# Kernel optimization log

Measured on AMD Instinct MI355X. Metric: run time of the kernel, lower is better.

The kernel has to match this reference:

```python
import jax, jax.numpy as jnp
import numpy as np

EPS = 0.5  # energy-relaxation learning rate (epsilon in __init__)


def rho(s):
    return jnp.clip(s, 0.0, 1.0)


def setup_inputs() -> dict:
    key = jax.random.key(0)
    k_x, k_w1, k_w2 = jax.random.split(key, 3)
    B, I, H, O = 8192, 1024, 128, 1000
    x = jax.random.uniform(k_x, (B, I), dtype=jnp.float32)
    hidden0 = jnp.zeros((B, H), dtype=jnp.float32)
    output0 = jnp.zeros((B, O), dtype=jnp.float32)
    b_in = jnp.zeros((I,), dtype=jnp.float32)
    b_h = jnp.zeros((H,), dtype=jnp.float32)
    b_o = jnp.zeros((O,), dtype=jnp.float32)
    # xavier_uniform: U(-a, a), a = sqrt(6 / (fan_in + fan_out))
    a1 = np.sqrt(6.0 / (I + H)).astype(np.float32)
    a2 = np.sqrt(6.0 / (H + O)).astype(np.float32)
    W1 = jax.random.uniform(k_w1, (I, H), minval=-a1, maxval=a1, dtype=jnp.float32)
    W2 = jax.random.uniform(k_w2, (H, O), minval=-a2, maxval=a2, dtype=jnp.float32)
    return {"x": x, "hidden0": hidden0, "output0": output0,
            "b_in": b_in, "b_h": b_h, "b_o": b_o,
            "W1": W1, "W2": W2, "n_iterations": 30}


def reference(x, hidden0, output0, b_in, b_h, b_o, W1, W2, n_iterations):
    # Hopfield-style energy summed over the batch (beta=0 / free phase):
    # E = 0.5*sum rho(s)^2 - sum rho(s).b - sum rho(pre) W rho(post)
    def energy(h, o):
        rx, rh, ro = rho(x), rho(h), rho(o)
        sq = 0.5 * ((rx * rx).sum() + (rh * rh).sum() + (ro * ro).sum())
        lin = -(rx @ b_in).sum() - (rh @ b_h).sum() - (ro @ b_o).sum()
        quad = -jnp.einsum('bi,ih,bh->', rx, W1, rh) \
               - jnp.einsum('bh,ho,bo->', rh, W2, ro)
        return sq + lin + quad

    grad_e = jax.grad(energy, argnums=(0, 1))

    def step(carry, _):
        h, o = carry
        gh, go = grad_e(h, o)
        h = jnp.clip(h - EPS * gh, 0.0, 1.0)
        o = jnp.clip(o - EPS * go, 0.0, 1.0)
        return (h, o), None

    (h, o), _ = jax.lax.scan(step, (hidden0, output0), None, length=n_iterations)
    return jax.nn.log_softmax(o, axis=1)
```

## Files before the change

kernel.cpp:

```cpp
#include <hip/hip_runtime.h>
#include <hip/hip_bf16.h>

typedef __bf16 bf16_t;
typedef __bf16 bf16x4_t __attribute__((ext_vector_type(4)));
typedef __bf16 bf16x8 __attribute__((ext_vector_type(8)));
typedef float f32x16 __attribute__((ext_vector_type(16)));

#define EPS 0.5f
#define MFMA32(a, b, c) __builtin_amdgcn_mfma_f32_32x32x16_bf16(a, b, c, 0, 0, 0)

__global__ __launch_bounds__(256) void prep_weights(
    const float* __restrict__ W1, const float* __restrict__ W2,
    bf16_t* __restrict__ W1t, bf16_t* __restrict__ W2B, bf16_t* __restrict__ W2T) {
  int idx = blockIdx.x * 256 + threadIdx.x;
  if (idx < 131072) {
    { int j = idx >> 10, i = idx & 1023; W1t[idx] = (bf16_t)W1[i * 128 + j]; }
    { int e = idx & 7, l = (idx >> 3) & 63, s = (idx >> 9) & 63, jt = idx >> 15;
      int j = jt * 32 + (l & 31), k = s * 16 + (l >> 5) * 8 + e;
      W2B[idx] = (bf16_t)((k < 1000) ? W2[j * 1000 + k] : 0.f); }
    { int e = idx & 7, l = (idx >> 3) & 63, js = (idx >> 9) & 7, kt = idx >> 12;
      int k = kt * 32 + (l & 31), j = js * 16 + (l >> 5) * 8 + e;
      W2T[idx] = (bf16_t)((k < 1000) ? W2[j * 1000 + k] : 0.f); }
  }
}

__global__ __launch_bounds__(256) void gemm_A(
    const float* __restrict__ x, const bf16_t* __restrict__ W1t,
    float* __restrict__ A) {
  int lane = threadIdx.x & 63, w = threadIdx.x >> 6;
  int lo = lane & 31, hi = lane >> 5;
  int row0 = blockIdx.x * 32;
  f32x16 acc = {};
  int kg = hi * 8;
  const float* xrow = x + (size_t)(row0 + lo) * 1024 + kg;
  const bf16_t* b0 = W1t + ((w * 32 + lo) << 10) + kg;
#pragma unroll 4
  for (int ks = 0; ks < 64; ++ks) {
    float xv[8];
    *(float4*)&xv[0] = *(const float4*)(xrow + ks * 16);
    *(float4*)&xv[4] = *(const float4*)(xrow + ks * 16 + 4);
    bf16x8 a;
#pragma unroll
    for (int i = 0; i < 8; ++i) a[i] = (bf16_t)xv[i];
    bf16x8 f0 = *(const bf16x8*)(b0 + ks * 16);
    acc = MFMA32(a, f0, acc);
  }
#pragma unroll
  for (int reg = 0; reg < 16; ++reg) {
    int r = (reg & 3) + 8 * (reg >> 2) + 4 * hi;
    A[(size_t)(row0 + r) * 128 + w * 32 + lo] = acc[reg];
  }
}

__device__ __forceinline__ bf16x4_t upd4(bf16x4_t v4, const float* u) {
  bf16x4_t n4;
#pragma unroll
  for (int r = 0; r < 4; ++r) {
    float v = (float)v4[r];
    float g = __builtin_fmaf(v, v, -v);
    float st = (g == 0.f) ? 0.25f : 0.5f;
    float n = __builtin_fmaf(-st, v - u[r], v);
    n4[r] = (bf16_t)__builtin_amdgcn_fmed3f(n, 0.f, 1.f);
  }
  return n4;
}

__global__ __launch_bounds__(1024, 4) void eqprop(
    const float* __restrict__ h0, const float* __restrict__ o0,
    const float* __restrict__ b_h, const float* __restrict__ b_o,
    const float* __restrict__ A, const bf16_t* __restrict__ W2B,
    const bf16_t* __restrict__ W2T, const int* __restrict__ nit,
    float* __restrict__ out) {
  __shared__ __align__(16) char o_raw[131072];
  __shared__ __align__(16) char h_raw[16384];
  __shared__ float bo_lds[1024];

  const int tid = threadIdx.x, lane = tid & 63, w = tid >> 6;
  const int lo = lane & 31, hi = lane >> 5;
  const int row0 = blockIdx.x * 32;

  for (int idx = tid; idx < 32768; idx += 1024) {
    int b = idx >> 10, k = idx & 1023;
    float v = (k < 1000) ? o0[(size_t)(row0 + b) * 1000 + k] : 0.f;
    int ad = ((k >> 4) << 10) + ((((k >> 3) & 1) << 5) + b) * 16 + ((k & 7) << 1);
    *(bf16_t*)(o_raw + ad) = (bf16_t)v;
  }
  for (int idx = tid; idx < 4096; idx += 1024) {
    int b = idx >> 7, j = idx & 127;
    int ad = ((j >> 4) << 10) + ((((j >> 3) & 1) << 5) + b) * 16 + ((j & 7) << 1);
    *(bf16_t*)(h_raw + ad) = (bf16_t)h0[(size_t)(row0 + b) * 128 + j];
  }
  bo_lds[tid] = (tid < 1000) ? b_o[tid] : 0.f;

  const int T = nit[0];
  int p = 0;
  __syncthreads();

  if (w < 4) {
    const int jt = w;
    const bf16_t* WB = W2B + (size_t)jt * 32768 + lane * 8;
#define CW(s) (*(const bf16x8*)(WB + (s) * 512))
    bf16x8 wres[16];
#pragma unroll
    for (int s = 0; s < 16; ++s) wres[s] = CW(s);
    const char* obase = o_raw + lane * 16;

    for (int t = 0; t < T; ++t) {
      const char* obP = obase + (p << 16);
#define OF(s) (*(const bf16x8*)(obP + (s) * 1024))
      f32x16 acc = {};
#pragma unroll
      for (int s = 0; s < 16; ++s) acc = MFMA32(wres[s], OF(s), acc);
      bf16x8 cs0[4], cs1[4];
      cs0[0] = CW(16); cs0[1] = CW(17); cs0[2] = CW(18); cs0[3] = CW(19);
#pragma unroll 1
      for (int c = 0; c < 12; ++c) {
        const int s0 = 16 + c * 4;
        if ((c & 1) == 0) {
          if (c < 11) {
            cs1[0] = CW(s0 + 4); cs1[1] = CW(s0 + 5);
            cs1[2] = CW(s0 + 6); cs1[3] = CW(s0 + 7);
          }
          acc = MFMA32(cs0[0], OF(s0 + 0), acc);
          acc = MFMA32(cs0[1], OF(s0 + 1), acc);
          acc = MFMA32(cs0[2], OF(s0 + 2), acc);
          acc = MFMA32(cs0[3], OF(s0 + 3), acc);
        } else {
          if (c < 11) {
            cs0[0] = CW(s0 + 4); cs0[1] = CW(s0 + 5);
            cs0[2] = CW(s0 + 6); cs0[3] = CW(s0 + 7);
          }
          acc = MFMA32(cs1[0], OF(s0 + 0), acc);
          acc = MFMA32(cs1[1], OF(s0 + 1), acc);
          acc = MFMA32(cs1[2], OF(s0 + 2), acc);
          acc = MFMA32(cs1[3], OF(s0 + 3), acc);
        }
      }
      const char* hrd = h_raw + (p << 13) + lo * 16 + hi * 8;
      char* hwr = h_raw + ((p ^ 1) << 13) + lo * 16 + hi * 8;
#pragma unroll
      for (int q = 0; q < 4; ++q) {
        const int jb = jt * 32 + q * 8 + 4 * hi;
        const int boff = (jt * 2 + (q >> 1)) * 1024 + (q & 1) * 512;
        float av[4], bh[4], u[4];
        *(float4*)av = *(const float4*)(A + (size_t)(row0 + lo) * 128 + jb);
        *(float4*)bh = *(const float4*)(b_h + jb);
#pragma unroll
        for (int r = 0; r < 4; ++r) u[r] = av[r] + bh[r] + acc[q * 4 + r];
        bf16x4_t v4 = *(const bf16x4_t*)(hrd + boff);
        *(bf16x4_t*)(hwr + boff) = upd4(v4, u);
      }
      __syncthreads();
      p ^= 1;
    }
  } else {
    const int wd = w - 4;
    const int kt0 = (wd < 8) ? wd * 3 : 24 + (wd - 8) * 2;
    const int nkt = (wd < 8) ? 3 : 2;
    const bf16_t* WT = W2T + (size_t)kt0 * 4096 + lane * 8;
#define DW(f) (*(const bf16x8*)(WT + (f) * 512))
    bf16x8 wres[8];
#pragma unroll
    for (int f = 0; f < 8; ++f) wres[f] = DW(f);
    const char* hbase = h_raw + lane * 16;
    const char* obase = o_raw + lo * 16 + hi * 8;

    for (int t = 0; t < T; ++t) {
      const char* hbP = hbase + (p << 13);
      bf16x8 hf[8];
#pragma unroll
      for (int js = 0; js < 8; ++js)
        hf[js] = *(const bf16x8*)(hbP + js * 1024);
      const char* ord = obase + (p << 16);
      char* owr = o_raw + lo * 16 + hi * 8 + ((p ^ 1) << 16);

#pragma unroll 1
      for (int kl = 0; kl < nkt; ++kl) {
        const int kt = kt0 + kl;
        f32x16 acc = {};
        if (kl == 0) {
#pragma unroll
          for (int js = 0; js < 8; ++js) acc = MFMA32(wres[js], hf[js], acc);
        } else {
          bf16x8 s0 = DW(kl * 8 + 0), s1 = DW(kl * 8 + 1);
          bf16x8 s2 = DW(kl * 8 + 2), s3 = DW(kl * 8 + 3);
          bf16x8 s4 = DW(kl * 8 + 4), s5 = DW(kl * 8 + 5);
          bf16x8 s6 = DW(kl * 8 + 6), s7 = DW(kl * 8 + 7);
          acc = MFMA32(s0, hf[0], acc);
          acc = MFMA32(s1, hf[1], acc);
          acc = MFMA32(s2, hf[2], acc);
          acc = MFMA32(s3, hf[3], acc);
          acc = MFMA32(s4, hf[4], acc);
          acc = MFMA32(s5, hf[5], acc);
          acc = MFMA32(s6, hf[6], acc);
          acc = MFMA32(s7, hf[7], acc);
        }
#pragma unroll
        for (int q = 0; q < 4; ++q) {
          const int boff = (kt * 2 + (q >> 1)) * 1024 + (q & 1) * 512;
          float bo4[4], u[4];
          *(float4*)bo4 = *(const float4*)(bo_lds + kt * 32 + q * 8 + 4 * hi);
#pragma unroll
          for (int r = 0; r < 4; ++r) u[r] = bo4[r] + acc[q * 4 + r];
          bf16x4_t v4 = *(const bf16x4_t*)(ord + boff);
          *(bf16x4_t*)(owr + boff) = upd4(v4, u);
        }
      }
      __syncthreads();
      p ^= 1;
    }
  }
  __syncthreads();

  const char* of = o_raw + (p << 16);
  for (int row = w * 2; row < w * 2 + 2; ++row) {
    float m = -1e30f;
    for (int k = lane; k < 1000; k += 64) {
      int ad = ((k >> 4) << 10) + ((((k >> 3) & 1) << 5) + row) * 16 + ((k & 7) << 1);
      m = fmaxf(m, (float)*(const bf16_t*)(of + ad));
    }
#pragma unroll
    for (int s = 32; s > 0; s >>= 1) m = fmaxf(m, __shfl_xor(m, s));
    float sum = 0.f;
    for (int k = lane; k < 1000; k += 64) {
      int ad = ((k >> 4) << 10) + ((((k >> 3) & 1) << 5) + row) * 16 + ((k & 7) << 1);
      sum += expf((float)*(const bf16_t*)(of + ad) - m);
    }
#pragma unroll
    for (int s = 32; s > 0; s >>= 1) sum += __shfl_xor(sum, s);
    float lse = m + logf(sum);
    for (int k = lane; k < 1000; k += 64) {
      int ad = ((k >> 4) << 10) + ((((k >> 3) & 1) << 5) + row) * 16 + ((k & 7) << 1);
      out[(size_t)(row0 + row) * 1000 + k] =
          (float)*(const bf16_t*)(of + ad) - lse;
    }
  }
}

extern "C" void kernel_launch(void* const* d_in, const int* in_sizes, int n_in,
                              void* d_out, int out_size, void* d_ws, size_t ws_size,
                              hipStream_t stream) {
  const float* x   = (const float*)d_in[0];
  const float* h0  = (const float*)d_in[1];
  const float* o0  = (const float*)d_in[2];
  const float* b_h = (const float*)d_in[4];
  const float* b_o = (const float*)d_in[5];
  const float* W1  = (const float*)d_in[6];
  const float* W2  = (const float*)d_in[7];
  const int*   nit = (const int*)d_in[8];
  float* out = (float*)d_out;

  char* ws = (char*)d_ws;
  float*  A   = (float*)ws;
  bf16_t* W1t = (bf16_t*)(ws + 4194304);
  bf16_t* W2B = (bf16_t*)(ws + 4194304 + 262144);
  bf16_t* W2T = (bf16_t*)(ws + 4194304 + 524288);

  prep_weights<<<512, 256, 0, stream>>>(W1, W2, W1t, W2B, W2T);
  gemm_A<<<256, 256, 0, stream>>>(x, W1t, A);
  eqprop<<<256, 1024, 0, stream>>>(h0, o0, b_h, b_o, A, W2B, W2T, nit, out);
}
```

Before: 263.5 us.

## Single-buffer output state in LDS and stage leftover W2T tiles in shared memory

```diff
diff --git a/kernel.cpp b/kernel.cpp
--- a/kernel.cpp
+++ b/kernel.cpp
@@ -6,7 +6,6 @@
 typedef __bf16 bf16x8 __attribute__((ext_vector_type(8)));
 typedef float f32x16 __attribute__((ext_vector_type(16)));
 
-#define EPS 0.5f
 #define MFMA32(a, b, c) __builtin_amdgcn_mfma_f32_32x32x16_bf16(a, b, c, 0, 0, 0)
 
 __global__ __launch_bounds__(256) void prep_weights(
@@ -71,8 +70,9 @@
     const float* __restrict__ A, const bf16_t* __restrict__ W2B,
     const bf16_t* __restrict__ W2T, const int* __restrict__ nit,
     float* __restrict__ out) {
-  __shared__ __align__(16) char o_raw[131072];
+  __shared__ __align__(16) char o_raw[65536];
   __shared__ __align__(16) char h_raw[16384];
+  __shared__ __align__(16) char wlds[65536];
   __shared__ float bo_lds[1024];
 
   const int tid = threadIdx.x, lane = tid & 63, w = tid >> 6;
@@ -90,6 +90,9 @@
     int ad = ((j >> 4) << 10) + ((((j >> 3) & 1) << 5) + b) * 16 + ((j & 7) << 1);
     *(bf16_t*)(h_raw + ad) = (bf16_t)h0[(size_t)(row0 + b) * 128 + j];
   }
+#pragma unroll
+  for (int c = 0; c < 4; ++c)
+    ((uint4*)wlds)[tid + c * 1024] = ((const uint4*)(W2T + 98304))[tid + c * 1024];
   bo_lds[tid] = (tid < 1000) ? b_o[tid] : 0.f;
 
   const int T = nit[0];
@@ -104,10 +107,9 @@
 #pragma unroll
     for (int s = 0; s < 16; ++s) wres[s] = CW(s);
     const char* obase = o_raw + lane * 16;
+#define OF(s) (*(const bf16x8*)(obase + (s) * 1024))
 
     for (int t = 0; t < T; ++t) {
-      const char* obP = obase + (p << 16);
-#define OF(s) (*(const bf16x8*)(obP + (s) * 1024))
       f32x16 acc = {};
 #pragma unroll
       for (int s = 0; s < 16; ++s) acc = MFMA32(wres[s], OF(s), acc);
@@ -151,80 +153,97 @@
         *(bf16x4_t*)(hwr + boff) = upd4(v4, u);
       }
       __syncthreads();
+      __syncthreads();
       p ^= 1;
     }
   } else {
     const int wd = w - 4;
-    const int kt0 = (wd < 8) ? wd * 3 : 24 + (wd - 8) * 2;
-    const int nkt = (wd < 8) ? 3 : 2;
-    const bf16_t* WT = W2T + (size_t)kt0 * 4096 + lane * 8;
-#define DW(f) (*(const bf16x8*)(WT + (f) * 512))
-    bf16x8 wres[8];
-#pragma unroll
-    for (int f = 0; f < 8; ++f) wres[f] = DW(f);
+    const bool has3 = (wd < 8);
+    const int ktA = has3 ? 2 * wd : 16 + 2 * (wd - 8);
+    const int ktB = ktA + 1;
+    const bf16_t* WTa = W2T + (size_t)(ktA * 8) * 512 + lane * 8;
+    bf16x8 wres[16];
+#pragma unroll
+    for (int f = 0; f < 16; ++f) wres[f] = *(const bf16x8*)(WTa + f * 512);
     const char* hbase = h_raw + lane * 16;
-    const char* obase = o_raw + lo * 16 + hi * 8;
+    const char* ob = o_raw + lo * 16 + hi * 8;
+    char* ow = o_raw + lo * 16 + hi * 8;
+    const char* wl = wlds + wd * 8192 + lane * 16;
+
+#define MAKE_NO(kt, accv, no)                                              \
+  {                                                                        \
+    _Pragma("unroll") for (int q = 0; q < 4; ++q) {                        \
+      const int boff = ((kt) * 2 + (q >> 1)) * 1024 + (q & 1) * 512;       \
+      float u[4];                                                          \
+      *(float4*)u = *(const float4*)(bo_lds + (kt) * 32 + q * 8 + 4 * hi); \
+      u[0] += accv[q * 4 + 0]; u[1] += accv[q * 4 + 1];                    \
+      u[2] += accv[q * 4 + 2]; u[3] += accv[q * 4 + 3];                    \
+      bf16x4_t v4 = *(const bf16x4_t*)(ob + boff);                         \
+      no[q] = upd4(v4, u);                                                 \
+    }                                                                      \
+  }
+#define STORE_NO(kt, no)                                                   \
+  {                                                                        \
+    _Pragma("unroll") for (int q = 0; q < 4; ++q) {                        \
+      const int boff = ((kt) * 2 + (q >> 1)) * 1024 + (q & 1) * 512;       \
+      *(bf16x4_t*)(ow + boff) = no[q];                                     \
+    }                                                                      \
+  }
 
     for (int t = 0; t < T; ++t) {
-      const char* hbP = hbase + (p << 13);
-      bf16x8 hf[8];
-#pragma unroll
-      for (int js = 0; js < 8; ++js)
-        hf[js] = *(const bf16x8*)(hbP + js * 1024);
-      const char* ord = obase + (p << 16);
-      char* owr = o_raw + lo * 16 + hi * 8 + ((p ^ 1) << 16);
-
-#pragma unroll 1
-      for (int kl = 0; kl < nkt; ++kl) {
-        const int kt = kt0 + kl;
+      const char* hp = hbase + (p << 13);
+      bf16x4_t noA[4], noB[4];
+      {
         f32x16 acc = {};
-        if (kl == 0) {
-#pragma unroll
-          for (int js = 0; js < 8; ++js) acc = MFMA32(wres[js], hf[js], acc);
-        } else {
-          bf16x8 s0 = DW(kl * 8 + 0), s1 = DW(kl * 8 + 1);
-          bf16x8 s2 = DW(kl * 8 + 2), s3 = DW(kl * 8 + 3);
-          bf16x8 s4 = DW(kl * 8 + 4), s5 = DW(kl * 8 + 5);
-          bf16x8 s6 = DW(kl * 8 + 6), s7 = DW(kl * 8 + 7);
-          acc = MFMA32(s0, hf[0], acc);
-          acc = MFMA32(s1, hf[1], acc);
-          acc = MFMA32(s2, hf[2], acc);
-          acc = MFMA32(s3, hf[3], acc);
-          acc = MFMA32(s4, hf[4], acc);
-          acc = MFMA32(s5, hf[5], acc);
-          acc = MFMA32(s6, hf[6], acc);
-          acc = MFMA32(s7, hf[7], acc);
-        }
-#pragma unroll
-        for (int q = 0; q < 4; ++q) {
-          const int boff = (kt * 2 + (q >> 1)) * 1024 + (q & 1) * 512;
-          float bo4[4], u[4];
-          *(float4*)bo4 = *(const float4*)(bo_lds + kt * 32 + q * 8 + 4 * hi);
-#pragma unroll
-          for (int r = 0; r < 4; ++r) u[r] = bo4[r] + acc[q * 4 + r];
-          bf16x4_t v4 = *(const bf16x4_t*)(ord + boff);
-          *(bf16x4_t*)(owr + boff) = upd4(v4, u);
-        }
-      }
+#pragma unroll
+        for (int js = 0; js < 8; ++js) {
+          bf16x8 hf = *(const bf16x8*)(hp + js * 1024);
+          acc = MFMA32(wres[js], hf, acc);
+        }
+        MAKE_NO(ktA, acc, noA);
+      }
+      {
+        f32x16 acc = {};
+#pragma unroll
+        for (int js = 0; js < 8; ++js) {
+          bf16x8 hf = *(const bf16x8*)(hp + js * 1024);
+          acc = MFMA32(wres[8 + js], hf, acc);
+        }
+        MAKE_NO(ktB, acc, noB);
+      }
+      __syncthreads();
+      if (has3) {
+        f32x16 acc = {};
+#pragma unroll
+        for (int js = 0; js < 8; ++js) {
+          bf16x8 wf = *(const bf16x8*)(wl + js * 1024);
+          bf16x8 hf = *(const bf16x8*)(hp + js * 1024);
+          acc = MFMA32(wf, hf, acc);
+        }
+        bf16x4_t noC[4];
+        MAKE_NO(24 + wd, acc, noC);
+        STORE_NO(24 + wd, noC);
+      }
+      STORE_NO(ktA, noA);
+      STORE_NO(ktB, noB);
       __syncthreads();
       p ^= 1;
     }
   }
   __syncthreads();
 
-  const char* of = o_raw + (p << 16);
   for (int row = w * 2; row < w * 2 + 2; ++row) {
     float m = -1e30f;
     for (int k = lane; k < 1000; k += 64) {
       int ad = ((k >> 4) << 10) + ((((k >> 3) & 1) << 5) + row) * 16 + ((k & 7) << 1);
-      m = fmaxf(m, (float)*(const bf16_t*)(of + ad));
+      m = fmaxf(m, (float)*(const bf16_t*)(o_raw + ad));
     }
 #pragma unroll
     for (int s = 32; s > 0; s >>= 1) m = fmaxf(m, __shfl_xor(m, s));
     float sum = 0.f;
     for (int k = lane; k < 1000; k += 64) {
       int ad = ((k >> 4) << 10) + ((((k >> 3) & 1) << 5) + row) * 16 + ((k & 7) << 1);
-      sum += expf((float)*(const bf16_t*)(of + ad) - m);
+      sum += expf((float)*(const bf16_t*)(o_raw + ad) - m);
     }
 #pragma unroll
     for (int s = 32; s > 0; s >>= 1) sum += __shfl_xor(sum, s);
@@ -232,7 +251,7 @@
     for (int k = lane; k < 1000; k += 64) {
       int ad = ((k >> 4) << 10) + ((((k >> 3) & 1) << 5) + row) * 16 + ((k & 7) << 1);
       out[(size_t)(row0 + row) * 1000 + k] =
-          (float)*(const bf16_t*)(of + ad) - lse;
+          (float)*(const bf16_t*)(o_raw + ad) - lse;
     }
   }
 }
```

Result: slower. 517.5 us (+96.4%).

## Halve eqprop block to 512 threads with larger register-resident weight slices

Applied to the files above, without the earlier changes.

```diff
diff --git a/kernel.cpp b/kernel.cpp
--- a/kernel.cpp
+++ b/kernel.cpp
@@ -6,7 +6,6 @@
 typedef __bf16 bf16x8 __attribute__((ext_vector_type(8)));
 typedef float f32x16 __attribute__((ext_vector_type(16)));
 
-#define EPS 0.5f
 #define MFMA32(a, b, c) __builtin_amdgcn_mfma_f32_32x32x16_bf16(a, b, c, 0, 0, 0)
 
 __global__ __launch_bounds__(256) void prep_weights(
@@ -65,32 +64,33 @@
   return n4;
 }
 
-__global__ __launch_bounds__(1024, 4) void eqprop(
+__global__ __launch_bounds__(512, 2) void eqprop(
     const float* __restrict__ h0, const float* __restrict__ o0,
     const float* __restrict__ b_h, const float* __restrict__ b_o,
     const float* __restrict__ A, const bf16_t* __restrict__ W2B,
     const bf16_t* __restrict__ W2T, const int* __restrict__ nit,
     float* __restrict__ out) {
-  __shared__ __align__(16) char o_raw[131072];
-  __shared__ __align__(16) char h_raw[16384];
+  __shared__ __align__(16) char ob[2][65536];
+  __shared__ __align__(16) char hb[2][8192];
   __shared__ float bo_lds[1024];
 
   const int tid = threadIdx.x, lane = tid & 63, w = tid >> 6;
   const int lo = lane & 31, hi = lane >> 5;
   const int row0 = blockIdx.x * 32;
 
-  for (int idx = tid; idx < 32768; idx += 1024) {
+  for (int idx = tid; idx < 32768; idx += 512) {
     int b = idx >> 10, k = idx & 1023;
     float v = (k < 1000) ? o0[(size_t)(row0 + b) * 1000 + k] : 0.f;
     int ad = ((k >> 4) << 10) + ((((k >> 3) & 1) << 5) + b) * 16 + ((k & 7) << 1);
-    *(bf16_t*)(o_raw + ad) = (bf16_t)v;
-  }
-  for (int idx = tid; idx < 4096; idx += 1024) {
+    *(bf16_t*)(&ob[0][0] + ad) = (bf16_t)v;
+  }
+  for (int idx = tid; idx < 4096; idx += 512) {
     int b = idx >> 7, j = idx & 127;
     int ad = ((j >> 4) << 10) + ((((j >> 3) & 1) << 5) + b) * 16 + ((j & 7) << 1);
-    *(bf16_t*)(h_raw + ad) = (bf16_t)h0[(size_t)(row0 + b) * 128 + j];
-  }
-  bo_lds[tid] = (tid < 1000) ? b_o[tid] : 0.f;
+    *(bf16_t*)(&hb[0][0] + ad) = (bf16_t)h0[(size_t)(row0 + b) * 128 + j];
+  }
+  for (int idx = tid; idx < 1024; idx += 512)
+    bo_lds[idx] = (idx < 1000) ? b_o[idx] : 0.f;
 
   const int T = nit[0];
   int p = 0;
@@ -100,24 +100,32 @@
     const int jt = w;
     const bf16_t* WB = W2B + (size_t)jt * 32768 + lane * 8;
 #define CW(s) (*(const bf16x8*)(WB + (s) * 512))
-    bf16x8 wres[16];
-#pragma unroll
-    for (int s = 0; s < 16; ++s) wres[s] = CW(s);
-    const char* obase = o_raw + lane * 16;
+    bf16x8 wres[32];
+#pragma unroll
+    for (int s = 0; s < 32; ++s) wres[s] = CW(s);
+    float uh[16];
+#pragma unroll
+    for (int q = 0; q < 4; ++q) {
+      const int jb = jt * 32 + q * 8 + 4 * hi;
+      float4 a4 = *(const float4*)(A + (size_t)(row0 + lo) * 128 + jb);
+      float4 b4 = *(const float4*)(b_h + jb);
+      uh[q * 4 + 0] = a4.x + b4.x; uh[q * 4 + 1] = a4.y + b4.y;
+      uh[q * 4 + 2] = a4.z + b4.z; uh[q * 4 + 3] = a4.w + b4.w;
+    }
 
     for (int t = 0; t < T; ++t) {
-      const char* obP = obase + (p << 16);
-#define OF(s) (*(const bf16x8*)(obP + (s) * 1024))
+      const char* obase = &ob[p][0] + lane * 16;
+#define OF(s) (*(const bf16x8*)(obase + (s) * 1024))
       f32x16 acc = {};
 #pragma unroll
-      for (int s = 0; s < 16; ++s) acc = MFMA32(wres[s], OF(s), acc);
+      for (int s = 0; s < 32; ++s) acc = MFMA32(wres[s], OF(s), acc);
       bf16x8 cs0[4], cs1[4];
-      cs0[0] = CW(16); cs0[1] = CW(17); cs0[2] = CW(18); cs0[3] = CW(19);
+      cs0[0] = CW(32); cs0[1] = CW(33); cs0[2] = CW(34); cs0[3] = CW(35);
 #pragma unroll 1
-      for (int c = 0; c < 12; ++c) {
-        const int s0 = 16 + c * 4;
+      for (int c = 0; c < 8; ++c) {
+        const int s0 = 32 + c * 4;
         if ((c & 1) == 0) {
-          if (c < 11) {
+          if (c < 7) {
             cs1[0] = CW(s0 + 4); cs1[1] = CW(s0 + 5);
             cs1[2] = CW(s0 + 6); cs1[3] = CW(s0 + 7);
           }
@@ -126,7 +134,7 @@
           acc = MFMA32(cs0[2], OF(s0 + 2), acc);
           acc = MFMA32(cs0[3], OF(s0 + 3), acc);
         } else {
-          if (c < 11) {
+          if (c < 7) {
             cs0[0] = CW(s0 + 4); cs0[1] = CW(s0 + 5);
             cs0[2] = CW(s0 + 6); cs0[3] = CW(s0 + 7);
           }
@@ -136,17 +144,14 @@
           acc = MFMA32(cs1[3], OF(s0 + 3), acc);
         }
       }
-      const char* hrd = h_raw + (p << 13) + lo * 16 + hi * 8;
-      char* hwr = h_raw + ((p ^ 1) << 13) + lo * 16 + hi * 8;
+      const char* hrd = &hb[p][0] + lo * 16 + hi * 8;
+      char* hwr = &hb[p ^ 1][0] + lo * 16 + hi * 8;
 #pragma unroll
       for (int q = 0; q < 4; ++q) {
-        const int jb = jt * 32 + q * 8 + 4 * hi;
         const int boff = (jt * 2 + (q >> 1)) * 1024 + (q & 1) * 512;
-        float av[4], bh[4], u[4];
-        *(float4*)av = *(const float4*)(A + (size_t)(row0 + lo) * 128 + jb);
-        *(float4*)bh = *(const float4*)(b_h + jb);
-#pragma unroll
-        for (int r = 0; r < 4; ++r) u[r] = av[r] + bh[r] + acc[q * 4 + r];
+        float u[4];
+#pragma unroll
+        for (int r = 0; r < 4; ++r) u[r] = uh[q * 4 + r] + acc[q * 4 + r];
         bf16x4_t v4 = *(const bf16x4_t*)(hrd + boff);
         *(bf16x4_t*)(hwr + boff) = upd4(v4, u);
       }
@@ -155,53 +160,71 @@
     }
   } else {
     const int wd = w - 4;
-    const int kt0 = (wd < 8) ? wd * 3 : 24 + (wd - 8) * 2;
-    const int nkt = (wd < 8) ? 3 : 2;
-    const bf16_t* WT = W2T + (size_t)kt0 * 4096 + lane * 8;
-#define DW(f) (*(const bf16x8*)(WT + (f) * 512))
-    bf16x8 wres[8];
-#pragma unroll
-    for (int f = 0; f < 8; ++f) wres[f] = DW(f);
-    const char* hbase = h_raw + lane * 16;
-    const char* obase = o_raw + lo * 16 + hi * 8;
+    const int ktbase = wd * 8;
+    const bf16_t* WT = W2T + (size_t)ktbase * 4096 + lane * 8;
+    bf16x8 wres[32];
+#pragma unroll
+    for (int f = 0; f < 32; ++f) wres[f] = *(const bf16x8*)(WT + f * 512);
 
     for (int t = 0; t < T; ++t) {
-      const char* hbP = hbase + (p << 13);
+      const char* hp = &hb[p][0] + lane * 16;
+      const char* ord = &ob[p][0] + lo * 16 + hi * 8;
+      char* owr = &ob[p ^ 1][0] + lo * 16 + hi * 8;
       bf16x8 hf[8];
 #pragma unroll
       for (int js = 0; js < 8; ++js)
-        hf[js] = *(const bf16x8*)(hbP + js * 1024);
-      const char* ord = obase + (p << 16);
-      char* owr = o_raw + lo * 16 + hi * 8 + ((p ^ 1) << 16);
-
+        hf[js] = *(const bf16x8*)(hp + js * 1024);
+
+#pragma unroll
+      for (int i = 0; i < 4; ++i) {
+        f32x16 acc = {};
+#pragma unroll
+        for (int js = 0; js < 8; ++js)
+          acc = MFMA32(wres[i * 8 + js], hf[js], acc);
+        const int kt = ktbase + i;
+#pragma unroll
+        for (int q = 0; q < 4; ++q) {
+          const int boff = (kt * 2 + (q >> 1)) * 1024 + (q & 1) * 512;
+          float u[4];
+          *(float4*)u = *(const float4*)(bo_lds + kt * 32 + q * 8 + 4 * hi);
+#pragma unroll
+          for (int r = 0; r < 4; ++r) u[r] += acc[q * 4 + r];
+          bf16x4_t v4 = *(const bf16x4_t*)(ord + boff);
+          *(bf16x4_t*)(owr + boff) = upd4(v4, u);
+        }
+      }
 #pragma unroll 1
-      for (int kl = 0; kl < nkt; ++kl) {
-        const int kt = kt0 + kl;
+      for (int kl = 4; kl < 8; ++kl) {
+        const bf16_t* wt = WT + (size_t)kl * 4096;
         f32x16 acc = {};
-        if (kl == 0) {
-#pragma unroll
-          for (int js = 0; js < 8; ++js) acc = MFMA32(wres[js], hf[js], acc);
-        } else {
-          bf16x8 s0 = DW(kl * 8 + 0), s1 = DW(kl * 8 + 1);
-          bf16x8 s2 = DW(kl * 8 + 2), s3 = DW(kl * 8 + 3);
-          bf16x8 s4 = DW(kl * 8 + 4), s5 = DW(kl * 8 + 5);
-          bf16x8 s6 = DW(kl * 8 + 6), s7 = DW(kl * 8 + 7);
+        {
+          bf16x8 s0 = *(const bf16x8*)(wt + 0 * 512);
+          bf16x8 s1 = *(const bf16x8*)(wt + 1 * 512);
+          bf16x8 s2 = *(const bf16x8*)(wt + 2 * 512);
+          bf16x8 s3 = *(const bf16x8*)(wt + 3 * 512);
           acc = MFMA32(s0, hf[0], acc);
           acc = MFMA32(s1, hf[1], acc);
           acc = MFMA32(s2, hf[2], acc);
           acc = MFMA32(s3, hf[3], acc);
+        }
+        {
+          bf16x8 s4 = *(const bf16x8*)(wt + 4 * 512);
+          bf16x8 s5 = *(const bf16x8*)(wt + 5 * 512);
+          bf16x8 s6 = *(const bf16x8*)(wt + 6 * 512);
+          bf16x8 s7 = *(const bf16x8*)(wt + 7 * 512);
           acc = MFMA32(s4, hf[4], acc);
           acc = MFMA32(s5, hf[5], acc);
           acc = MFMA32(s6, hf[6], acc);
           acc = MFMA32(s7, hf[7], acc);
         }
+        const int kt = ktbase + kl;
 #pragma unroll
         for (int q = 0; q < 4; ++q) {
           const int boff = (kt * 2 + (q >> 1)) * 1024 + (q & 1) * 512;
-          float bo4[4], u[4];
-          *(float4*)bo4 = *(const float4*)(bo_lds + kt * 32 + q * 8 + 4 * hi);
-#pragma unroll
-          for (int r = 0; r < 4; ++r) u[r] = bo4[r] + acc[q * 4 + r];
+          float u[4];
+          *(float4*)u = *(const float4*)(bo_lds + kt * 32 + q * 8 + 4 * hi);
+#pragma unroll
+          for (int r = 0; r < 4; ++r) u[r] += acc[q * 4 + r];
           bf16x4_t v4 = *(const bf16x4_t*)(ord + boff);
           *(bf16x4_t*)(owr + boff) = upd4(v4, u);
         }
@@ -212,8 +235,8 @@
   }
   __syncthreads();
 
-  const char* of = o_raw + (p << 16);
-  for (int row = w * 2; row < w * 2 + 2; ++row) {
+  const char* of = &ob[p][0];
+  for (int row = w * 4; row < w * 4 + 4; ++row) {
     float m = -1e30f;
     for (int k = lane; k < 1000; k += 64) {
       int ad = ((k >> 4) << 10) + ((((k >> 3) & 1) << 5) + row) * 16 + ((k & 7) << 1);
@@ -258,5 +281,5 @@
 
   prep_weights<<<512, 256, 0, stream>>>(W1, W2, W1t, W2B, W2T);
   gemm_A<<<256, 256, 0, stream>>>(x, W1t, A);
-  eqprop<<<256, 1024, 0, stream>>>(h0, o0, b_h, b_o, A, W2B, W2T, nit, out);
-}
+  eqprop<<<256, 512, 0, stream>>>(h0, o0, b_h, b_o, A, W2B, W2T, nit, out);
+}
```

After: 249.0 us. 5.5% less time.
